# Optimization experiments

Hardware: AMD Instinct MI355X
Metric: run time of the kernel (lower is better)

Reference implementation:

```python
import jax, jax.numpy as jnp
import numpy as np

TWO_PI = 2.0 * np.pi
D_IN, N, P, C, BATCH = 784, 1024, 128, 10, 256
T, BETA, K_COUP, A_ANC = 0.5, 2.0, 1.0, 0.08
OMEGA_ANC = TWO_PI * 200.0
N_STEPS = 16  # fixed-grid RK4 steps over [0, T]


def setup_inputs() -> dict:
    key = jax.random.key(0)
    k0, k1, k2, k3 = jax.random.split(key, 4)
    x = jax.random.normal(k0, (BATCH, D_IN), dtype=jnp.float32)
    W_enc = jax.random.normal(k1, (N, D_IN), dtype=jnp.float32) * (1.0 / np.sqrt(D_IN))
    b_enc = jnp.zeros((N,), dtype=jnp.float32)
    xi = jax.random.uniform(k2, (P, N), dtype=jnp.float32) * TWO_PI  # memory patterns
    W_out = jax.random.normal(k3, (C, 2 * N), dtype=jnp.float32) * (1.0 / np.sqrt(2 * N))
    b_out = jnp.zeros((C,), dtype=jnp.float32)
    return {"x": x, "W_enc": W_enc, "b_enc": b_enc, "xi": xi, "W_out": W_out, "b_out": b_out}


def _dphi(t, phi, xi):
    # phi: (B, N), xi: (P, N) -> diff: (B, P, N)
    diff = phi[:, None, :] - xi[None, :, :]
    m = jnp.cos(diff).sum(-1)                               # (B, P) overlaps
    w = jax.nn.softmax(BETA * m / N, axis=-1)               # (B, P)
    coupling = jnp.einsum('bp,bpn->bn', w, jnp.sin(diff))   # (B, N)
    return K_COUP * coupling + A_ANC * jnp.sin(OMEGA_ANC * t - phi)


def reference(x, W_enc, b_enc, xi, W_out, b_out):
    # Encoder: phi0 in (0, 2pi)
    phi0 = TWO_PI * jax.nn.sigmoid(x @ W_enc.T + b_enc)
    dt = T / N_STEPS

    def step(phi, t):
        k1 = _dphi(t, phi, xi)
        k2 = _dphi(t + 0.5 * dt, phi + 0.5 * dt * k1, xi)
        k3 = _dphi(t + 0.5 * dt, phi + 0.5 * dt * k2, xi)
        k4 = _dphi(t + dt, phi + dt * k3, xi)
        return phi + (dt / 6.0) * (k1 + 2.0 * k2 + 2.0 * k3 + k4), None

    ts = jnp.arange(N_STEPS, dtype=jnp.float32) * dt
    phi_T, _ = jax.lax.scan(step, phi0, ts)
    # Readout on [cos, sin] features
    feats = jnp.concatenate([jnp.cos(phi_T), jnp.sin(phi_T)], axis=-1)
    return feats @ W_out.T + b_out
```

## Files before the change

kernel.cpp:

```cpp
#include <hip/hip_runtime.h>
#include <math.h>


typedef __attribute__((ext_vector_type(4))) float f32x4;
typedef __attribute__((ext_vector_type(2))) float f32x2;
typedef __attribute__((ext_vector_type(8))) short bf16x8;
typedef __attribute__((ext_vector_type(4))) unsigned short u16x4;
typedef __attribute__((ext_vector_type(2))) long i64x2;

struct TCons { float s[64]; float c[64]; };

__device__ __forceinline__ unsigned short f2bf(float f) {
  unsigned u = __builtin_bit_cast(unsigned, f);
  return (unsigned short)((u + 0x7FFFu + ((u >> 16) & 1u)) >> 16);
}
__device__ __forceinline__ long pk8fp8(const float* v) {
  unsigned lo = __builtin_amdgcn_cvt_pk_fp8_f32(v[0], v[1], 0, false);
  lo = __builtin_amdgcn_cvt_pk_fp8_f32(v[2], v[3], lo, true);
  unsigned hi = __builtin_amdgcn_cvt_pk_fp8_f32(v[4], v[5], 0, false);
  hi = __builtin_amdgcn_cvt_pk_fp8_f32(v[6], v[7], hi, true);
  return (long)lo | ((long)hi << 32);
}

#define A1_OFF    0
#define MBUF_OFF  16384
#define W_OFF     20608
#define ZP_OFF    22656
#define XST_OFF   22672
#define T2L_OFF   29344
#define RED_OFF   29344
#define LDS_BYTES 160416

__global__
__attribute__((amdgpu_flat_work_group_size(1024, 1024), amdgpu_waves_per_eu(4, 4)))
void phasenn_kernel(
    const float* __restrict__ x, const float* __restrict__ W_enc,
    const float* __restrict__ b_enc, const float* __restrict__ xi,
    const float* __restrict__ W_out, const float* __restrict__ b_out,
    float* __restrict__ dout, char* __restrict__ wsb, TCons tc)
{
  __shared__ __align__(16) char smem[LDS_BYTES];

  const int tid  = threadIdx.x;
  const int bk   = blockIdx.x;
  const int w    = tid >> 6;
  const int lane = tid & 63;
  const int q    = lane >> 4;
  const int b16  = lane & 15;
  const int g    = b16 >> 2;
  const int row4 = b16 & 3;
  const int xr5  = row4 * 5;

  char* T1g = wsb;
  char* T2g = wsb + (256 << 10);

  if (tid < 4) *(unsigned*)(smem + ZP_OFF + tid*4) = 0;

  {
    const int row = tid >> 7, dg = tid & 127;
    if (row < 4 && dg < 100) {
      bf16x8 fr = {0,0,0,0,0,0,0,0};
      if (dg < 98) {
        f32x4 v0 = *(const f32x4*)(x + (bk*4 + row)*784 + dg*8);
        f32x4 v1 = *(const f32x4*)(x + (bk*4 + row)*784 + dg*8 + 4);
        #pragma unroll
        for (int i = 0; i < 8; ++i) fr[i] = (short)f2bf(i < 4 ? v0[i] : v1[i-4]);
      }
      *(bf16x8*)(smem + XST_OFF + row*1664 + (((dg ^ row) & 127) << 4)) = fr;
    }
  }

  if (w < 8) {
    const int p = w*16 + b16;
    for (int f = 0; f < 32; ++f) {
      const int n0 = f*32 + q*8;
      f32x4 v0 = *(const f32x4*)(xi + p*1024 + n0);
      f32x4 v1 = *(const f32x4*)(xi + p*1024 + n0 + 4);
      float cv[8], sv[8];
      #pragma unroll
      for (int i = 0; i < 8; ++i) {
        float xv = (i < 4) ? v0[i] : v1[i-4];
        sv[i] = __sinf(xv); cv[i] = __cosf(xv);
      }
      i64x2 pr; pr[0] = pk8fp8(cv); pr[1] = pk8fp8(sv);
      *(i64x2*)(T1g + (size_t)((w*32 + f)*64 + lane)*16) = pr;
    }
  } else {
    const int w2 = w - 8;
    const bool toLds = (w2 < 4);
    for (int f = 0; f < 32; ++f) {
      const int ct = w2*8 + (f >> 2), pt2 = f & 3;
      const int n = ct*16 + b16;
      float cv[8], sv[8];
      #pragma unroll
      for (int i = 0; i < 8; ++i) {
        float xv = xi[(pt2*32 + q*8 + i)*1024 + n];
        sv[i] = __sinf(xv); cv[i] = __cosf(xv);
      }
      i64x2 pr; pr[0] = pk8fp8(cv); pr[1] = pk8fp8(sv);
      if (toLds)
        *(i64x2*)(smem + T2L_OFF + (size_t)((ct*4 + pt2)*64 + lane)*16) = pr;
      else
        *(i64x2*)(T2g + (size_t)((ct*4 + pt2)*64 + lane)*16) = pr;
    }
  }
  __syncthreads();

  float p0[4], ka[4], pwv[4];
  {
    f32x4 pac[4] = {{0,0,0,0},{0,0,0,0},{0,0,0,0},{0,0,0,0}};
    for (int kt = 0; kt < 25; ++kt) {
      const char* baddr =
          smem + XST_OFF + row4*1664 + ((((kt*4 + q) ^ row4) & 127) << 4);
      bf16x8 bfr = *(const bf16x8*)baddr;
      const int d = kt*32 + q*8;
      #pragma unroll
      for (int j = 0; j < 4; ++j) {
        bf16x8 afr = {0,0,0,0,0,0,0,0};
        if (d < 784) {
          const int n = (w*4 + j)*16 + b16;
          f32x4 v0 = *(const f32x4*)(W_enc + n*784 + d);
          f32x4 v1 = *(const f32x4*)(W_enc + n*784 + d + 4);
          #pragma unroll
          for (int i = 0; i < 8; ++i) afr[i] = (short)f2bf(i < 4 ? v0[i] : v1[i-4]);
        }
        pac[j] = __builtin_amdgcn_mfma_f32_16x16x32_bf16(afr, bfr, pac[j], 0, 0, 0);
      }
    }
    f32x4 pc = (g==0) ? pac[0] : (g==1) ? pac[1] : (g==2) ? pac[2] : pac[3];
    #pragma unroll
    for (int r = 0; r < 4; ++r) {
      const int n = (w*4 + g)*16 + q*4 + r;
      float ph = 6.283185307179586f / (1.0f + __expf(-(pc[r] + b_enc[n])));
      p0[r] = ph; pwv[r] = ph; ka[r] = 0.0f;
    }
  }

  const float dtf = 0.03125f, half = 0.015625f;
  const float sixth = (float)(0.03125/6.0);

  for (int e = 0; e < 64; ++e) {
    float csv[4], snv[4];
    {
      #pragma unroll
      for (int r = 0; r < 4; ++r) {
        snv[r] = __sinf(pwv[r]);
        csv[r] = __cosf(pwv[r]);
      }
      unsigned cp = __builtin_amdgcn_cvt_pk_fp8_f32(csv[0], csv[1], 0, false);
      cp = __builtin_amdgcn_cvt_pk_fp8_f32(csv[2], csv[3], cp, true);
      unsigned sp = __builtin_amdgcn_cvt_pk_fp8_f32(snv[0], snv[1], 0, false);
      sp = __builtin_amdgcn_cvt_pk_fp8_f32(snv[2], snv[3], sp, true);
      const int u = (w*4 + g)*2 + (q >> 1);
      char* base = smem + A1_OFF + row4*2048 + ((q & 1) << 2);
      *(unsigned*)(base + ((u ^ xr5) << 3))        = cp;
      *(unsigned*)(base + 1024 + ((u ^ xr5) << 3)) = sp;
    }
    __syncthreads();

    {
      const int pt = w & 7, kh = w >> 3;
      f32x4 accC = {0.f, 0.f, 0.f, 0.f}, accS = {0.f, 0.f, 0.f, 0.f};
      const char* t1b = T1g + (size_t)((pt*32 + kh*16)*64 + lane)*16;
      const char* a1b = smem + A1_OFF + row4*2048;
      #pragma unroll 8
      for (int i2 = 0; i2 < 16; ++i2) {
        const int ktc = kh*16 + i2;
        i64x2 af = *(const i64x2*)(t1b + (size_t)i2*1024);
        long bc = *(const long*)(a1b + (((ktc*4 + q) ^ xr5) << 3));
        long bs = *(const long*)(a1b + 1024 + (((ktc*4 + q) ^ xr5) << 3));
        accC = __builtin_amdgcn_mfma_f32_16x16x32_fp8_fp8(af[0], bc, accC, 0, 0, 0);
        accS = __builtin_amdgcn_mfma_f32_16x16x32_fp8_fp8(af[1], bs, accS, 0, 0, 0);
      }
      if (b16 < 4) {
        f32x4 acc = accC + accS;
        *(f32x4*)(smem + MBUF_OFF + kh*2112 + b16*528 + ((pt*16 + q*4) << 2)) = acc;
      }
    }
    __syncthreads();

    if (w < 4) {
      const char* mb = smem + MBUF_OFF + w*528 + lane*8;
      f32x2 u0 = *(const f32x2*)(mb);
      f32x2 u1 = *(const f32x2*)(mb + 2112);
      float e0 = __expf((u0[0] + u1[0]) * 0.001953125f);
      float e1 = __expf((u0[1] + u1[1]) * 0.001953125f);
      float s = e0 + e1;
      #pragma unroll
      for (int off = 1; off < 64; off <<= 1) s += __shfl_xor(s, off, 64);
      const float inv64 = 64.0f / s;
      unsigned pk = __builtin_amdgcn_cvt_pk_fp8_f32(e0*inv64, e1*inv64, 0, false);
      const int pp = lane*2, u = pp >> 3;
      #pragma unroll
      for (int t = 0; t < 4; ++t) {
        const int rr = w + t*4;
        *(unsigned short*)(smem + W_OFF + rr*128 + ((u ^ rr) << 3) + (pp & 7)) =
            (unsigned short)pk;
      }
    }
    __syncthreads();

    {
      const float swt = tc.s[e], cwt = tc.c[e];
      const int st = e & 3;
      long wfr[4];
      #pragma unroll
      for (int pt2 = 0; pt2 < 4; ++pt2)
        wfr[pt2] = *(const long*)(smem + W_OFF + b16*128 + (((pt2*4 + q) ^ b16) << 3));
      f32x4 aC[4] = {{0,0,0,0},{0,0,0,0},{0,0,0,0},{0,0,0,0}};
      f32x4 aS[4] = {{0,0,0,0},{0,0,0,0},{0,0,0,0},{0,0,0,0}};
      if (w < 8) {
        const char* t2Lb = smem + T2L_OFF + (size_t)(w*16*64 + lane)*16;
        #pragma unroll
        for (int c = 0; c < 4; ++c)
          #pragma unroll
          for (int pt2 = 0; pt2 < 4; ++pt2) {
            i64x2 tf = *(const i64x2*)(t2Lb + (size_t)(c*4 + pt2)*1024);
            aC[c] = __builtin_amdgcn_mfma_f32_16x16x32_fp8_fp8(tf[0], wfr[pt2], aC[c], 0,0,0);
            aS[c] = __builtin_amdgcn_mfma_f32_16x16x32_fp8_fp8(tf[1], wfr[pt2], aS[c], 0,0,0);
          }
      } else {
        const char* t2b = T2g + (size_t)(w*16*64 + lane)*16;
        #pragma unroll
        for (int c = 0; c < 4; ++c)
          #pragma unroll
          for (int pt2 = 0; pt2 < 4; ++pt2) {
            i64x2 tf = *(const i64x2*)(t2b + (size_t)(c*4 + pt2)*1024);
            aC[c] = __builtin_amdgcn_mfma_f32_16x16x32_fp8_fp8(tf[0], wfr[pt2], aC[c], 0,0,0);
            aS[c] = __builtin_amdgcn_mfma_f32_16x16x32_fp8_fp8(tf[1], wfr[pt2], aS[c], 0,0,0);
          }
      }
      f32x4 vC4 = (g==0) ? aC[0] : (g==1) ? aC[1] : (g==2) ? aC[2] : aC[3];
      f32x4 vS4 = (g==0) ? aS[0] : (g==1) ? aS[1] : (g==2) ? aS[2] : aS[3];
      #pragma unroll
      for (int r = 0; r < 4; ++r) {
        float s_ = snv[r];
        float c_ = csv[r];
        float kv = (s_*vC4[r] - c_*vS4[r]) * 0.015625f
                 + 0.08f*(swt*c_ - cwt*s_);
        if (st == 0)      { ka[r]  = kv;           pwv[r] = p0[r] + kv*half; }
        else if (st == 1) { ka[r] += 2.0f*kv;      pwv[r] = p0[r] + kv*half; }
        else if (st == 2) { ka[r] += 2.0f*kv;      pwv[r] = p0[r] + kv*dtf;  }
        else { ka[r] += kv; p0[r] += ka[r]*sixth; pwv[r] = p0[r]; }
      }
    }
  }

  __syncthreads();
  {
    u16x4 cp, sp;
    #pragma unroll
    for (int r = 0; r < 4; ++r) {
      float ph = p0[r];
      cp[r] = f2bf(__cosf(ph)); sp[r] = f2bf(__sinf(ph));
    }
    const int cj = (w*4 + g)*2 + (q >> 1);
    char* base = smem + A1_OFF + row4*4096 + ((q & 1) << 3);
    *(u16x4*)(base + ((cj ^ row4) << 4))        = cp;
    *(u16x4*)(base + ((cj ^ row4) << 4) + 2048) = sp;
  }
  __syncthreads();
  {
    f32x4 acc = {0.f, 0.f, 0.f, 0.f};
    #pragma unroll
    for (int i2 = 0; i2 < 4; ++i2) {
      const int kt = w*4 + i2;
      const int k = kt*32 + q*8;
      bf16x8 afr = {0,0,0,0,0,0,0,0};
      if (b16 < 10) {
        f32x4 v0 = *(const f32x4*)(W_out + b16*2048 + k);
        f32x4 v1 = *(const f32x4*)(W_out + b16*2048 + k + 4);
        #pragma unroll
        for (int i = 0; i < 8; ++i) afr[i] = (short)f2bf(i < 4 ? v0[i] : v1[i-4]);
      }
      const char* baddr = (b16 < 4)
          ? (smem + A1_OFF + b16*4096 + ((((kt*4 + q) ^ b16) & 255) << 4))
          : (smem + ZP_OFF);
      bf16x8 bfr = *(const bf16x8*)baddr;
      acc = __builtin_amdgcn_mfma_f32_16x16x32_bf16(afr, bfr, acc, 0, 0, 0);
    }
    *(f32x4*)(smem + RED_OFF + ((w*64 + lane) << 4)) = acc;
  }
  __syncthreads();
  if (tid < 64) {
    f32x4 s = {0.f, 0.f, 0.f, 0.f};
    #pragma unroll
    for (int w2 = 0; w2 < 16; ++w2)
      s += *(const f32x4*)(smem + RED_OFF + ((w2*64 + tid) << 4));
    const int b = tid & 15, q2 = tid >> 4;
    if (b < 4) {
      #pragma unroll
      for (int r = 0; r < 4; ++r) {
        const int cl = q2*4 + r;
        if (cl < 10)
          dout[(bk*4 + b)*10 + cl] = s[r] + b_out[cl];
      }
    }
  }
}

extern "C" void kernel_launch(void* const* d_in, const int* in_sizes, int n_in,
                              void* d_out, int out_size, void* d_ws, size_t ws_size,
                              hipStream_t stream) {
  (void)in_sizes; (void)n_in; (void)ws_size; (void)out_size;
  const float* x     = (const float*)d_in[0];
  const float* W_enc = (const float*)d_in[1];
  const float* b_enc = (const float*)d_in[2];
  const float* xi    = (const float*)d_in[3];
  const float* W_out = (const float*)d_in[4];
  const float* b_out = (const float*)d_in[5];
  float* out = (float*)d_out;
  char* wsb = (char*)d_ws;

  TCons tc;
  const double OME = 2.0 * 3.14159265358979323846 * 200.0;
  const double dtd = 0.03125;
  const double co[4] = {0.0, 0.5, 0.5, 1.0};
  for (int e = 0; e < 64; ++e) {
    double t = ((double)(e >> 2) + co[e & 3]) * dtd;
    tc.s[e] = (float)sin(OME * t);
    tc.c[e] = (float)cos(OME * t);
  }

  phasenn_kernel<<<dim3(64), dim3(1024), 0, stream>>>(
      x, W_enc, b_enc, xi, W_out, b_out, out, wsb, tc);
}
```

Measured before the change: 432.8 us.

## Process two batch rows per block and launch 128 blocks

Halves the batch rows handled per workgroup from four to two and doubles the grid to 128 blocks, so more of the MI355X's compute units work on the serial RK4 loop. The freed LDS space holds more of the precomputed sin/cos(xi) fp8 tiles (36 column tiles instead of 32), which cuts global reads in the coupling matmul. In exchange, the MFMA tiles carry more padding per useful row, and each block repeats the xi table preparation and the encoder weight loads.

Measured after the change: 413.6 us. -4.5%, faster.

```diff
diff --git a/kernel.cpp b/kernel.cpp
--- a/kernel.cpp
+++ b/kernel.cpp
@@ -5,7 +5,7 @@
 typedef __attribute__((ext_vector_type(4))) float f32x4;
 typedef __attribute__((ext_vector_type(2))) float f32x2;
 typedef __attribute__((ext_vector_type(8))) short bf16x8;
-typedef __attribute__((ext_vector_type(4))) unsigned short u16x4;
+typedef __attribute__((ext_vector_type(2))) unsigned short u16x2;
 typedef __attribute__((ext_vector_type(2))) long i64x2;
 
 struct TCons { float s[64]; float c[64]; };
@@ -23,13 +23,13 @@
 }
 
 #define A1_OFF    0
-#define MBUF_OFF  16384
-#define W_OFF     20608
-#define ZP_OFF    22656
-#define XST_OFF   22672
-#define T2L_OFF   29344
-#define RED_OFF   29344
-#define LDS_BYTES 160416
+#define MBUF_OFF  8192
+#define W_OFF     10304
+#define ZP_OFF    10560
+#define XST_OFF   10576
+#define T2L_OFF   13904
+#define RED_OFF   13904
+#define LDS_BYTES 161360
 
 __global__
 __attribute__((amdgpu_flat_work_group_size(1024, 1024), amdgpu_waves_per_eu(4, 4)))
@@ -47,9 +47,10 @@
   const int lane = tid & 63;
   const int q    = lane >> 4;
   const int b16  = lane & 15;
-  const int g    = b16 >> 2;
-  const int row4 = b16 & 3;
-  const int xr5  = row4 * 5;
+  const int row2 = b16 & 1;
+  const int j4   = b16 >> 2;
+  const int rp   = (b16 >> 1) & 1;
+  const int swz  = row2 * 5;
 
   char* T1g = wsb;
   char* T2g = wsb + (256 << 10);
@@ -58,11 +59,11 @@
 
   {
     const int row = tid >> 7, dg = tid & 127;
-    if (row < 4 && dg < 100) {
+    if (row < 2 && dg < 100) {
       bf16x8 fr = {0,0,0,0,0,0,0,0};
       if (dg < 98) {
-        f32x4 v0 = *(const f32x4*)(x + (bk*4 + row)*784 + dg*8);
-        f32x4 v1 = *(const f32x4*)(x + (bk*4 + row)*784 + dg*8 + 4);
+        f32x4 v0 = *(const f32x4*)(x + (bk*2 + row)*784 + dg*8);
+        f32x4 v1 = *(const f32x4*)(x + (bk*2 + row)*784 + dg*8 + 4);
         #pragma unroll
         for (int i = 0; i < 8; ++i) fr[i] = (short)f2bf(i < 4 ? v0[i] : v1[i-4]);
       }
@@ -87,7 +88,6 @@
     }
   } else {
     const int w2 = w - 8;
-    const bool toLds = (w2 < 4);
     for (int f = 0; f < 32; ++f) {
       const int ct = w2*8 + (f >> 2), pt2 = f & 3;
       const int n = ct*16 + b16;
@@ -98,7 +98,7 @@
         sv[i] = __sinf(xv); cv[i] = __cosf(xv);
       }
       i64x2 pr; pr[0] = pk8fp8(cv); pr[1] = pk8fp8(sv);
-      if (toLds)
+      if (ct < 36)
         *(i64x2*)(smem + T2L_OFF + (size_t)((ct*4 + pt2)*64 + lane)*16) = pr;
       else
         *(i64x2*)(T2g + (size_t)((ct*4 + pt2)*64 + lane)*16) = pr;
@@ -106,12 +106,12 @@
   }
   __syncthreads();
 
-  float p0[4], ka[4], pwv[4];
+  float p0[2], ka[2], pwv[2];
   {
     f32x4 pac[4] = {{0,0,0,0},{0,0,0,0},{0,0,0,0},{0,0,0,0}};
     for (int kt = 0; kt < 25; ++kt) {
       const char* baddr =
-          smem + XST_OFF + row4*1664 + ((((kt*4 + q) ^ row4) & 127) << 4);
+          smem + XST_OFF + row2*1664 + ((((kt*4 + q) ^ row2) & 127) << 4);
       bf16x8 bfr = *(const bf16x8*)baddr;
       const int d = kt*32 + q*8;
       #pragma unroll
@@ -127,34 +127,33 @@
         pac[j] = __builtin_amdgcn_mfma_f32_16x16x32_bf16(afr, bfr, pac[j], 0, 0, 0);
       }
     }
-    f32x4 pc = (g==0) ? pac[0] : (g==1) ? pac[1] : (g==2) ? pac[2] : pac[3];
-    #pragma unroll
-    for (int r = 0; r < 4; ++r) {
-      const int n = (w*4 + g)*16 + q*4 + r;
-      float ph = 6.283185307179586f / (1.0f + __expf(-(pc[r] + b_enc[n])));
-      p0[r] = ph; pwv[r] = ph; ka[r] = 0.0f;
-    }
+    f32x4 pc = (j4==0) ? pac[0] : (j4==1) ? pac[1] : (j4==2) ? pac[2] : pac[3];
+    float vA = rp ? pc[2] : pc[0];
+    float vB = rp ? pc[3] : pc[1];
+    const int n0 = (w*4 + j4)*16 + q*4 + rp*2;
+    float ph0 = 6.283185307179586f / (1.0f + __expf(-(vA + b_enc[n0])));
+    float ph1 = 6.283185307179586f / (1.0f + __expf(-(vB + b_enc[n0 + 1])));
+    p0[0] = ph0; pwv[0] = ph0; ka[0] = 0.0f;
+    p0[1] = ph1; pwv[1] = ph1; ka[1] = 0.0f;
   }
 
   const float dtf = 0.03125f, half = 0.015625f;
   const float sixth = (float)(0.03125/6.0);
 
   for (int e = 0; e < 64; ++e) {
-    float csv[4], snv[4];
+    float csv[2], snv[2];
     {
       #pragma unroll
-      for (int r = 0; r < 4; ++r) {
+      for (int r = 0; r < 2; ++r) {
         snv[r] = __sinf(pwv[r]);
         csv[r] = __cosf(pwv[r]);
       }
       unsigned cp = __builtin_amdgcn_cvt_pk_fp8_f32(csv[0], csv[1], 0, false);
-      cp = __builtin_amdgcn_cvt_pk_fp8_f32(csv[2], csv[3], cp, true);
       unsigned sp = __builtin_amdgcn_cvt_pk_fp8_f32(snv[0], snv[1], 0, false);
-      sp = __builtin_amdgcn_cvt_pk_fp8_f32(snv[2], snv[3], sp, true);
-      const int u = (w*4 + g)*2 + (q >> 1);
-      char* base = smem + A1_OFF + row4*2048 + ((q & 1) << 2);
-      *(unsigned*)(base + ((u ^ xr5) << 3))        = cp;
-      *(unsigned*)(base + 1024 + ((u ^ xr5) << 3)) = sp;
+      const int u = (w*4 + j4)*2 + (q >> 1);
+      char* base = smem + A1_OFF + row2*2048 + ((q & 1) << 2) + rp*2;
+      *(unsigned short*)(base + ((u ^ swz) << 3))        = (unsigned short)cp;
+      *(unsigned short*)(base + 1024 + ((u ^ swz) << 3)) = (unsigned short)sp;
     }
     __syncthreads();
 
@@ -162,27 +161,27 @@
       const int pt = w & 7, kh = w >> 3;
       f32x4 accC = {0.f, 0.f, 0.f, 0.f}, accS = {0.f, 0.f, 0.f, 0.f};
       const char* t1b = T1g + (size_t)((pt*32 + kh*16)*64 + lane)*16;
-      const char* a1b = smem + A1_OFF + row4*2048;
+      const char* a1b = smem + A1_OFF + row2*2048;
       #pragma unroll 8
       for (int i2 = 0; i2 < 16; ++i2) {
         const int ktc = kh*16 + i2;
         i64x2 af = *(const i64x2*)(t1b + (size_t)i2*1024);
-        long bc = *(const long*)(a1b + (((ktc*4 + q) ^ xr5) << 3));
-        long bs = *(const long*)(a1b + 1024 + (((ktc*4 + q) ^ xr5) << 3));
+        long bc = *(const long*)(a1b + (((ktc*4 + q) ^ swz) << 3));
+        long bs = *(const long*)(a1b + 1024 + (((ktc*4 + q) ^ swz) << 3));
         accC = __builtin_amdgcn_mfma_f32_16x16x32_fp8_fp8(af[0], bc, accC, 0, 0, 0);
         accS = __builtin_amdgcn_mfma_f32_16x16x32_fp8_fp8(af[1], bs, accS, 0, 0, 0);
       }
-      if (b16 < 4) {
+      if (b16 < 2) {
         f32x4 acc = accC + accS;
-        *(f32x4*)(smem + MBUF_OFF + kh*2112 + b16*528 + ((pt*16 + q*4) << 2)) = acc;
+        *(f32x4*)(smem + MBUF_OFF + kh*1056 + b16*528 + ((pt*16 + q*4) << 2)) = acc;
       }
     }
     __syncthreads();
 
-    if (w < 4) {
+    if (w < 2) {
       const char* mb = smem + MBUF_OFF + w*528 + lane*8;
       f32x2 u0 = *(const f32x2*)(mb);
-      f32x2 u1 = *(const f32x2*)(mb + 2112);
+      f32x2 u1 = *(const f32x2*)(mb + 1056);
       float e0 = __expf((u0[0] + u1[0]) * 0.001953125f);
       float e1 = __expf((u0[1] + u1[1]) * 0.001953125f);
       float s = e0 + e1;
@@ -191,12 +190,8 @@
       const float inv64 = 64.0f / s;
       unsigned pk = __builtin_amdgcn_cvt_pk_fp8_f32(e0*inv64, e1*inv64, 0, false);
       const int pp = lane*2, u = pp >> 3;
-      #pragma unroll
-      for (int t = 0; t < 4; ++t) {
-        const int rr = w + t*4;
-        *(unsigned short*)(smem + W_OFF + rr*128 + ((u ^ rr) << 3) + (pp & 7)) =
-            (unsigned short)pk;
-      }
+      *(unsigned short*)(smem + W_OFF + w*128 + ((u ^ w) << 3) + (pp & 7)) =
+          (unsigned short)pk;
     }
     __syncthreads();
 
@@ -206,10 +201,10 @@
       long wfr[4];
       #pragma unroll
       for (int pt2 = 0; pt2 < 4; ++pt2)
-        wfr[pt2] = *(const long*)(smem + W_OFF + b16*128 + (((pt2*4 + q) ^ b16) << 3));
+        wfr[pt2] = *(const long*)(smem + W_OFF + row2*128 + (((pt2*4 + q) ^ row2) << 3));
       f32x4 aC[4] = {{0,0,0,0},{0,0,0,0},{0,0,0,0},{0,0,0,0}};
       f32x4 aS[4] = {{0,0,0,0},{0,0,0,0},{0,0,0,0},{0,0,0,0}};
-      if (w < 8) {
+      if (w < 9) {
         const char* t2Lb = smem + T2L_OFF + (size_t)(w*16*64 + lane)*16;
         #pragma unroll
         for (int c = 0; c < 4; ++c)
@@ -230,13 +225,16 @@
             aS[c] = __builtin_amdgcn_mfma_f32_16x16x32_fp8_fp8(tf[1], wfr[pt2], aS[c], 0,0,0);
           }
       }
-      f32x4 vC4 = (g==0) ? aC[0] : (g==1) ? aC[1] : (g==2) ? aC[2] : aC[3];
-      f32x4 vS4 = (g==0) ? aS[0] : (g==1) ? aS[1] : (g==2) ? aS[2] : aS[3];
-      #pragma unroll
-      for (int r = 0; r < 4; ++r) {
+      f32x4 c4 = (j4==0) ? aC[0] : (j4==1) ? aC[1] : (j4==2) ? aC[2] : aC[3];
+      f32x4 s4 = (j4==0) ? aS[0] : (j4==1) ? aS[1] : (j4==2) ? aS[2] : aS[3];
+      float vC[2], vS[2];
+      vC[0] = rp ? c4[2] : c4[0];  vC[1] = rp ? c4[3] : c4[1];
+      vS[0] = rp ? s4[2] : s4[0];  vS[1] = rp ? s4[3] : s4[1];
+      #pragma unroll
+      for (int r = 0; r < 2; ++r) {
         float s_ = snv[r];
         float c_ = csv[r];
-        float kv = (s_*vC4[r] - c_*vS4[r]) * 0.015625f
+        float kv = (s_*vC[r] - c_*vS[r]) * 0.015625f
                  + 0.08f*(swt*c_ - cwt*s_);
         if (st == 0)      { ka[r]  = kv;           pwv[r] = p0[r] + kv*half; }
         else if (st == 1) { ka[r] += 2.0f*kv;      pwv[r] = p0[r] + kv*half; }
@@ -248,16 +246,16 @@
 
   __syncthreads();
   {
-    u16x4 cp, sp;
+    u16x2 cp, sp;
     #pragma unroll
-    for (int r = 0; r < 4; ++r) {
+    for (int r = 0; r < 2; ++r) {
       float ph = p0[r];
       cp[r] = f2bf(__cosf(ph)); sp[r] = f2bf(__sinf(ph));
     }
-    const int cj = (w*4 + g)*2 + (q >> 1);
-    char* base = smem + A1_OFF + row4*4096 + ((q & 1) << 3);
-    *(u16x4*)(base + ((cj ^ row4) << 4))        = cp;
-    *(u16x4*)(base + ((cj ^ row4) << 4) + 2048) = sp;
+    const int cj = (w*4 + j4)*2 + (q >> 1);
+    char* base = smem + A1_OFF + row2*4096 + ((q & 1) << 3) + rp*4;
+    *(u16x2*)(base + ((cj ^ row2) << 4))        = cp;
+    *(u16x2*)(base + ((cj ^ row2) << 4) + 2048) = sp;
   }
   __syncthreads();
   {
@@ -273,7 +271,7 @@
         #pragma unroll
         for (int i = 0; i < 8; ++i) afr[i] = (short)f2bf(i < 4 ? v0[i] : v1[i-4]);
       }
-      const char* baddr = (b16 < 4)
+      const char* baddr = (b16 < 2)
           ? (smem + A1_OFF + b16*4096 + ((((kt*4 + q) ^ b16) & 255) << 4))
           : (smem + ZP_OFF);
       bf16x8 bfr = *(const bf16x8*)baddr;
@@ -288,12 +286,12 @@
     for (int w2 = 0; w2 < 16; ++w2)
       s += *(const f32x4*)(smem + RED_OFF + ((w2*64 + tid) << 4));
     const int b = tid & 15, q2 = tid >> 4;
-    if (b < 4) {
+    if (b < 2) {
       #pragma unroll
       for (int r = 0; r < 4; ++r) {
         const int cl = q2*4 + r;
         if (cl < 10)
-          dout[(bk*4 + b)*10 + cl] = s[r] + b_out[cl];
+          dout[(bk*2 + b)*10 + cl] = s[r] + b_out[cl];
       }
     }
   }
@@ -322,6 +320,6 @@
     tc.c[e] = (float)cos(OME * t);
   }
 
-  phasenn_kernel<<<dim3(64), dim3(1024), 0, stream>>>(
+  phasenn_kernel<<<dim3(128), dim3(1024), 0, stream>>>(
       x, W_enc, b_enc, xi, W_out, b_out, out, wsb, tc);
 }
```
